# Kernel tuning notes

Hardware: AMD Instinct MI355X
Metric: run time of the kernel (lower is better)

Reference implementation:

```python
import jax, jax.numpy as jnp
import numpy as np

T, H, I, E, Z = 4096, 1024, 512, 64, 16   # tokens, hidden, intermediate, routed experts, zero experts
TOP_K = 2
SCALE = 1.5        # routed_scaling_factor
CAP = 320


def setup_inputs() -> dict:
    key = jax.random.key(0)
    k1, k2, k3, k4, k5 = jax.random.split(key, 5)
    return {
        "hidden_states": jax.random.normal(k1, (T, H), dtype=jnp.float32),
        "router_w": jax.random.normal(k2, (E + Z, H), dtype=jnp.float32) * 0.02,
        "correction_bias": jnp.zeros((E + Z,), dtype=jnp.float32),
        "w_gate": jax.random.normal(k3, (E, H, I), dtype=jnp.float32) * 0.02,
        "w_up": jax.random.normal(k4, (E, H, I), dtype=jnp.float32) * 0.02,
        "w_down": jax.random.normal(k5, (E, I, H), dtype=jnp.float32) * 0.02,
    }


def _moe_forward(hidden_states, router_w, correction_bias, w_gate, w_up, w_down):
    n_tok = hidden_states.shape[0]
    # ---- Router (fp32 gemm) ----
    logits = hidden_states @ router_w.T                      # [T, E+Z]
    scores = jax.nn.sigmoid(logits)                          # DeepSeek-V3-style sigmoid gating
    biased = scores + correction_bias[None, :]
    _, top_idx = jax.lax.top_k(biased, TOP_K)                # [T, K] selection on biased scores
    top_w = jnp.take_along_axis(scores, top_idx, axis=-1)    # weights from unbiased scores, no renorm

    # ---- Zero (identity) experts: ids >= E return the input token ----
    is_zero = top_idx >= E                                   # [T, K]
    zero_out = (top_w * is_zero).sum(-1, keepdims=True) * hidden_states

    # ---- Routed expert dispatch (capacity-based grouped GEMM) ----
    flat_e = jnp.where(is_zero, 0, top_idx).reshape(-1)      # [T*K]
    flat_w = jnp.where(is_zero, 0.0, top_w).reshape(-1)      # [T*K]
    routed_mask = (~is_zero).reshape(-1)
    oh = jax.nn.one_hot(flat_e, E, dtype=jnp.int32) * routed_mask[:, None].astype(jnp.int32)
    pos = (jnp.cumsum(oh, axis=0) * oh).sum(-1) - 1          # rank within expert; -1 for zero-expert slots
    valid = (pos >= 0) & (pos < CAP)
    pos_c = jnp.where(valid, pos, CAP)                       # overflow/zero slots -> spill row CAP
    x_rep = jnp.repeat(hidden_states, TOP_K, axis=0)         # [T*K, H]
    buf = jnp.zeros((E, CAP + 1, hidden_states.shape[1]), dtype=hidden_states.dtype)
    buf = buf.at[flat_e, pos_c].set(x_rep)[:, :CAP]          # [E, CAP, H]

    # ---- Grouped SwiGLU experts ----
    g = jax.nn.silu(jnp.einsum('ech,ehi->eci', buf, w_gate)) * jnp.einsum('ech,ehi->eci', buf, w_up)
    out_e = jnp.einsum('eci,eih->ech', g, w_down)            # [E, CAP, H]

    # ---- Combine ----
    pos_g = jnp.where(valid, pos, 0)
    y = out_e[flat_e, pos_g] * (flat_w * valid)[:, None]     # [T*K, H]
    routed = y.reshape(n_tok, TOP_K, -1).sum(1)

    return (routed + zero_out) * SCALE                       # routed_scaling_factor applied on output


def reference(hidden_states, router_w, correction_bias, w_gate, w_up, w_down):
    return _moe_forward(hidden_states, router_w, correction_bias, w_gate, w_up, w_down)
```

## Files before the change

### kernel.cpp

```cpp
#include <hip/hip_runtime.h>
#include <hip/hip_bf16.h>
#include <stdint.h>


#define T_TOK 4096
#define HDIM  1024
#define IDIM  512
#define NE    64
#define NEZ   80
#define CAPE  320
#define SCALEF 1.5f

typedef __attribute__((ext_vector_type(8))) short bf16x8;
typedef __attribute__((ext_vector_type(4))) float floatx4;

static __device__ __forceinline__ unsigned short f2bf(float f) {
    unsigned int x = __float_as_uint(f);
    x += 0x7fffu + ((x >> 16) & 1u);
    return (unsigned short)(x >> 16);
}
static __device__ __forceinline__ float bf2f(unsigned short u) {
    return __uint_as_float(((unsigned int)u) << 16);
}
static __device__ __forceinline__ uint4 pack8(const float* f) {
    uint4 v;
    asm("v_cvt_pk_bf16_f32 %0, %1, %2" : "=v"(v.x) : "v"(f[0]), "v"(f[1]));
    asm("v_cvt_pk_bf16_f32 %0, %1, %2" : "=v"(v.y) : "v"(f[2]), "v"(f[3]));
    asm("v_cvt_pk_bf16_f32 %0, %1, %2" : "=v"(v.z) : "v"(f[4]), "v"(f[5]));
    asm("v_cvt_pk_bf16_f32 %0, %1, %2" : "=v"(v.w) : "v"(f[6]), "v"(f[7]));
    return v;
}
static __device__ __forceinline__ uint2 pack4(float4 f) {
    uint2 v;
    asm("v_cvt_pk_bf16_f32 %0, %1, %2" : "=v"(v.x) : "v"(f.x), "v"(f.y));
    asm("v_cvt_pk_bf16_f32 %0, %1, %2" : "=v"(v.y) : "v"(f.z), "v"(f.w));
    return v;
}

__global__ __launch_bounds__(256) void router_kernel(
    const float* __restrict__ hidden, const float* __restrict__ rw,
    const float* __restrict__ bias, int* __restrict__ cnt,
    int* __restrict__ slot_tok, float* __restrict__ w_routed,
    float* __restrict__ zc)
{
    __shared__ float sc[8][NEZ];
    __shared__ float sbias[NEZ];
    const int tid = threadIdx.x;
    const int w = tid >> 6, lane = tid & 63;
    const int t0 = blockIdx.x * 8 + w * 2;

    if (tid < NEZ) sbias[tid] = bias[tid];

    float4 xr[2][4];
#pragma unroll
    for (int tt = 0; tt < 2; ++tt)
#pragma unroll
        for (int j4 = 0; j4 < 4; ++j4)
            xr[tt][j4] = *(const float4*)&hidden[(size_t)(t0 + tt) * HDIM + lane * 16 + j4 * 4];

    for (int eb = 0; eb < NEZ; eb += 16) {
        float acc[2][16];
#pragma unroll
        for (int tt = 0; tt < 2; ++tt)
#pragma unroll
            for (int ee = 0; ee < 16; ++ee) acc[tt][ee] = 0.f;

#pragma unroll
        for (int ee = 0; ee < 16; ++ee) {
            const float* r = rw + (size_t)(eb + ee) * HDIM + lane * 16;
#pragma unroll
            for (int j4 = 0; j4 < 4; ++j4) {
                float4 rv = *(const float4*)&r[j4 * 4];
                acc[0][ee] += xr[0][j4].x * rv.x + xr[0][j4].y * rv.y
                            + xr[0][j4].z * rv.z + xr[0][j4].w * rv.w;
                acc[1][ee] += xr[1][j4].x * rv.x + xr[1][j4].y * rv.y
                            + xr[1][j4].z * rv.z + xr[1][j4].w * rv.w;
            }
        }
#pragma unroll
        for (int off = 32; off > 0; off >>= 1)
#pragma unroll
            for (int tt = 0; tt < 2; ++tt)
#pragma unroll
                for (int ee = 0; ee < 16; ++ee)
                    acc[tt][ee] += __shfl_xor(acc[tt][ee], off);

        if (lane == 0) {
#pragma unroll
            for (int tt = 0; tt < 2; ++tt)
#pragma unroll
                for (int ee = 0; ee < 16; ++ee)
                    sc[w * 2 + tt][eb + ee] = 1.f / (1.f + __expf(-acc[tt][ee]));
        }
    }
    __syncthreads();

    if (tid < 8) {
        const int t = blockIdx.x * 8 + tid;
        float b1 = -1e30f, b2 = -1e30f; int i1 = 0, i2 = 0;
        for (int e = 0; e < NEZ; ++e) {
            float b = sc[tid][e] + sbias[e];
            if (b > b1) { b2 = b1; i2 = i1; b1 = b; i1 = e; }
            else if (b > b2) { b2 = b; i2 = e; }
        }
        float z = 0.f;
        int idx2[2] = { i1, i2 };
        for (int k = 0; k < 2; ++k) {
            int e = idx2[k];
            float wgt = sc[tid][e];
            float wr = 0.f;
            if (e >= NE) {
                z += wgt;
            } else {
                int pos = atomicAdd(&cnt[e], 1);
                if (pos < CAPE) { slot_tok[e * CAPE + pos] = t * 2 + k; wr = wgt; }
            }
            w_routed[t * 2 + k] = wr;
        }
        zc[t] = z;
    }
}

#define GU_BG 4096
#define GU_BU 8192
__global__ __launch_bounds__(256, 2) void gateup_kernel(
    const float* __restrict__ hidden,
    const float* __restrict__ w_gate, const float* __restrict__ w_up,
    const int* __restrict__ cnt, const int* __restrict__ slot_tok,
    unsigned short* __restrict__ gbuf)
{
    const int e  = blockIdx.x;
    const int n0 = blockIdx.y * 128;
    const int m0 = blockIdx.z * 128;
    int cnt_e = cnt[e]; if (cnt_e > CAPE) cnt_e = CAPE;
    if (m0 >= cnt_e) return;

    __shared__ unsigned short lds[12288];
    __shared__ int sTok[128];

    const int tid = threadIdx.x;
    const int lane = tid & 63, wid = tid >> 6;
    const int ml = lane & 15, quad = lane >> 4;
    const int wm = wid >> 1, wn = wid & 1;

    if (tid < 128) {
        int r = m0 + tid;
        sTok[tid] = (r < cnt_e) ? (slot_tok[e * CAPE + r] >> 1) : 0;
    }
    __syncthreads();

    const int ak4 = tid & 7;
    const float* ha[4];
    int aoff[4];
#pragma unroll
    for (int p = 0; p < 4; ++p) {
        int arow = (tid >> 3) + 32 * p;
        aoff[p] = (arow >> 4) * 512 + ((ak4 >> 1) * 16 + (arow & 15)) * 8 + (ak4 & 1) * 4;
        ha[p] = hidden + (size_t)sTok[arow] * HDIM + ak4 * 4;
    }
    const int bn = tid & 127, bk = tid >> 7;
    const int boff0 = (bn >> 4) * 512 + ((bk * 2) * 16 + (bn & 15)) * 8;
    const int boff1 = boff0 + 128;

    const size_t ebase = (size_t)e * HDIM * IDIM;
    const float* wg_p = w_gate + ebase + (size_t)(bk * 16) * IDIM + n0 + bn;
    const float* wu_p = w_up   + ebase + (size_t)(bk * 16) * IDIM + n0 + bn;

    float4 aR[4];
    float  gR[16], uR[16];

#pragma unroll
    for (int p = 0; p < 4; ++p) aR[p] = *(const float4*)ha[p];
#pragma unroll
    for (int jj = 0; jj < 16; ++jj) {
        gR[jj] = wg_p[(size_t)jj * IDIM];
        uR[jj] = wu_p[(size_t)jj * IDIM];
    }

    floatx4 ag[4][4], au[4][4];
#pragma unroll
    for (int mt = 0; mt < 4; ++mt)
#pragma unroll
        for (int nt = 0; nt < 4; ++nt) {
            ag[mt][nt] = (floatx4){0.f, 0.f, 0.f, 0.f};
            au[mt][nt] = (floatx4){0.f, 0.f, 0.f, 0.f};
        }

    for (int kc = 0; kc < HDIM; kc += 32) {
        {
#pragma unroll
            for (int p = 0; p < 4; ++p)
                *(uint2*)&lds[aoff[p]] = pack4(aR[p]);
            *(uint4*)&lds[GU_BG + boff0] = pack8(gR);
            *(uint4*)&lds[GU_BG + boff1] = pack8(gR + 8);
            *(uint4*)&lds[GU_BU + boff0] = pack8(uR);
            *(uint4*)&lds[GU_BU + boff1] = pack8(uR + 8);
        }
        __syncthreads();

        if (kc + 32 < HDIM) {
            wg_p += (size_t)32 * IDIM; wu_p += (size_t)32 * IDIM;
#pragma unroll
            for (int p = 0; p < 4; ++p) { ha[p] += 32; aR[p] = *(const float4*)ha[p]; }
#pragma unroll
            for (int jj = 0; jj < 16; ++jj) {
                gR[jj] = wg_p[(size_t)jj * IDIM];
                uR[jj] = wu_p[(size_t)jj * IDIM];
            }
        }

        bf16x8 a[4], bg[4], bu[4];
#pragma unroll
        for (int mt = 0; mt < 4; ++mt)
            a[mt] = *(const bf16x8*)&lds[(wm * 4 + mt) * 512 + lane * 8];
#pragma unroll
        for (int nt = 0; nt < 4; ++nt) {
            bg[nt] = *(const bf16x8*)&lds[GU_BG + (wn * 4 + nt) * 512 + lane * 8];
            bu[nt] = *(const bf16x8*)&lds[GU_BU + (wn * 4 + nt) * 512 + lane * 8];
        }
#pragma unroll
        for (int mt = 0; mt < 4; ++mt)
#pragma unroll
            for (int nt = 0; nt < 4; ++nt) {
                ag[mt][nt] = __builtin_amdgcn_mfma_f32_16x16x32_bf16(a[mt], bg[nt], ag[mt][nt], 0, 0, 0);
                au[mt][nt] = __builtin_amdgcn_mfma_f32_16x16x32_bf16(a[mt], bu[nt], au[mt][nt], 0, 0, 0);
            }
        __syncthreads();
    }

#pragma unroll
    for (int mt = 0; mt < 4; ++mt) {
#pragma unroll
        for (int r4 = 0; r4 < 4; ++r4) {
            int gm = m0 + wm * 64 + mt * 16 + quad * 4 + r4;
            if (gm < cnt_e) {
                unsigned short* grow = gbuf + (size_t)(e * CAPE + gm) * IDIM + n0 + wn * 64;
#pragma unroll
                for (int nt = 0; nt < 4; ++nt) {
                    float g = ag[mt][nt][r4];
                    float u = au[mt][nt][r4];
                    float s = g / (1.f + __expf(-g));
                    grow[nt * 16 + ml] = f2bf(s * u);
                }
            }
        }
    }
}

#define DN_B 4096
__global__ __launch_bounds__(256, 2) void down_kernel(
    const unsigned short* __restrict__ gbuf, const float* __restrict__ w_down,
    const int* __restrict__ cnt, const int* __restrict__ slot_tok,
    unsigned short* __restrict__ y2)
{
    const int e  = blockIdx.x;
    const int n0 = blockIdx.y * 128;
    const int m0 = blockIdx.z * 128;
    int cnt_e = cnt[e]; if (cnt_e > CAPE) cnt_e = CAPE;
    if (m0 >= cnt_e) return;

    __shared__ unsigned short lds[8192];
    __shared__ int sSlot[128];

    const int tid = threadIdx.x;
    const int lane = tid & 63, wid = tid >> 6;
    const int ml = lane & 15, quad = lane >> 4;
    const int wm = wid >> 1, wn = wid & 1;

    if (tid < 128) {
        int r = m0 + tid;
        sSlot[tid] = (r < cnt_e) ? slot_tok[e * CAPE + r] : 0;
    }
    __syncthreads();

    const int au8 = tid & 3;
    const unsigned short* gp[2];
    int aoff[2];
#pragma unroll
    for (int p = 0; p < 2; ++p) {
        int arow = (tid >> 2) + 64 * p;
        aoff[p] = (arow >> 4) * 512 + (au8 * 16 + (arow & 15)) * 8;
        gp[p] = gbuf + (size_t)(e * CAPE + m0 + arow) * IDIM + au8 * 8;
    }
    const int bn = tid & 127, bk = tid >> 7;
    const int boff0 = (bn >> 4) * 512 + ((bk * 2) * 16 + (bn & 15)) * 8;
    const int boff1 = boff0 + 128;
    const float* wd_p = w_down + (size_t)e * IDIM * HDIM + (size_t)(bk * 16) * HDIM + n0 + bn;

    uint4 aR[2];
    float bR[16];

#pragma unroll
    for (int p = 0; p < 2; ++p) aR[p] = *(const uint4*)gp[p];
#pragma unroll
    for (int jj = 0; jj < 16; ++jj) bR[jj] = wd_p[(size_t)jj * HDIM];

    floatx4 acc[4][4];
#pragma unroll
    for (int mt = 0; mt < 4; ++mt)
#pragma unroll
        for (int nt = 0; nt < 4; ++nt)
            acc[mt][nt] = (floatx4){0.f, 0.f, 0.f, 0.f};

    for (int kc = 0; kc < IDIM; kc += 32) {
#pragma unroll
        for (int p = 0; p < 2; ++p)
            *(uint4*)&lds[aoff[p]] = aR[p];
        *(uint4*)&lds[DN_B + boff0] = pack8(bR);
        *(uint4*)&lds[DN_B + boff1] = pack8(bR + 8);
        __syncthreads();

        if (kc + 32 < IDIM) {
            wd_p += (size_t)32 * HDIM;
#pragma unroll
            for (int p = 0; p < 2; ++p) { gp[p] += 32; aR[p] = *(const uint4*)gp[p]; }
#pragma unroll
            for (int jj = 0; jj < 16; ++jj) bR[jj] = wd_p[(size_t)jj * HDIM];
        }

        bf16x8 a[4], b[4];
#pragma unroll
        for (int mt = 0; mt < 4; ++mt)
            a[mt] = *(const bf16x8*)&lds[(wm * 4 + mt) * 512 + lane * 8];
#pragma unroll
        for (int nt = 0; nt < 4; ++nt)
            b[nt] = *(const bf16x8*)&lds[DN_B + (wn * 4 + nt) * 512 + lane * 8];
#pragma unroll
        for (int mt = 0; mt < 4; ++mt)
#pragma unroll
            for (int nt = 0; nt < 4; ++nt)
                acc[mt][nt] = __builtin_amdgcn_mfma_f32_16x16x32_bf16(a[mt], b[nt], acc[mt][nt], 0, 0, 0);
        __syncthreads();
    }

#pragma unroll
    for (int mt = 0; mt < 4; ++mt) {
#pragma unroll
        for (int r4 = 0; r4 < 4; ++r4) {
            int lrow = wm * 64 + mt * 16 + quad * 4 + r4;
            if (m0 + lrow < cnt_e) {
                int slot = sSlot[lrow];
                unsigned short* yrow = y2 + (size_t)slot * HDIM + n0 + wn * 64;
#pragma unroll
                for (int nt = 0; nt < 4; ++nt)
                    yrow[nt * 16 + ml] = f2bf(acc[mt][nt][r4]);
            }
        }
    }
}

__global__ __launch_bounds__(256) void combine_kernel(
    const float* __restrict__ hidden, const unsigned short* __restrict__ y2,
    const float* __restrict__ w_routed, const float* __restrict__ zc,
    float* __restrict__ out)
{
    int gid = blockIdx.x * 256 + threadIdx.x;
    int t = gid >> 8;
    int h = (gid & 255) * 4;
    float4 x = *(const float4*)(hidden + (size_t)t * HDIM + h);
    float w0 = w_routed[t * 2 + 0];
    float w1 = w_routed[t * 2 + 1];
    float z  = zc[t];
    ushort4 ya = *(const ushort4*)(y2 + (size_t)(t * 2 + 0) * HDIM + h);
    ushort4 yb = *(const ushort4*)(y2 + (size_t)(t * 2 + 1) * HDIM + h);
    float4 o;
    o.x = SCALEF * (z * x.x + w0 * bf2f(ya.x) + w1 * bf2f(yb.x));
    o.y = SCALEF * (z * x.y + w0 * bf2f(ya.y) + w1 * bf2f(yb.y));
    o.z = SCALEF * (z * x.z + w0 * bf2f(ya.z) + w1 * bf2f(yb.z));
    o.w = SCALEF * (z * x.w + w0 * bf2f(ya.w) + w1 * bf2f(yb.w));
    *(float4*)(out + (size_t)t * HDIM + h) = o;
}

#define OFF_CNT   0
#define OFF_SLOT  4096
#define OFF_WR    (OFF_SLOT + NE * CAPE * 4)
#define OFF_ZC    (OFF_WR + T_TOK * 2 * 4)
#define OFF_GBUF  (OFF_ZC + T_TOK * 4)
#define OFF_Y2    (OFF_GBUF + (size_t)NE * CAPE * IDIM * 2)

extern "C" void kernel_launch(void* const* d_in, const int* in_sizes, int n_in,
                              void* d_out, int out_size, void* d_ws, size_t ws_size,
                              hipStream_t stream) {
    const float* hidden = (const float*)d_in[0];
    const float* rw     = (const float*)d_in[1];
    const float* bias   = (const float*)d_in[2];
    const float* w_gate = (const float*)d_in[3];
    const float* w_up   = (const float*)d_in[4];
    const float* w_down = (const float*)d_in[5];
    float* out = (float*)d_out;

    char* ws = (char*)d_ws;
    int*   cnt      = (int*)(ws + OFF_CNT);
    int*   slot_tok = (int*)(ws + OFF_SLOT);
    float* w_rt     = (float*)(ws + OFF_WR);
    float* zc       = (float*)(ws + OFF_ZC);
    unsigned short* gbuf = (unsigned short*)(ws + OFF_GBUF);
    unsigned short* y2   = (unsigned short*)(ws + OFF_Y2);

    hipMemsetAsync(cnt, 0, NE * sizeof(int), stream);

    router_kernel<<<T_TOK / 8, 256, 0, stream>>>(hidden, rw, bias, cnt, slot_tok, w_rt, zc);

    gateup_kernel<<<dim3(NE, IDIM / 128, (CAPE + 127) / 128), 256, 0, stream>>>(
        hidden, w_gate, w_up, cnt, slot_tok, gbuf);

    down_kernel<<<dim3(NE, HDIM / 128, (CAPE + 127) / 128), 256, 0, stream>>>(
        gbuf, w_down, cnt, slot_tok, y2);

    combine_kernel<<<(T_TOK * HDIM / 4) / 256, 256, 0, stream>>>(
        hidden, y2, w_rt, zc, out);
}
```

Baseline: 483.4 us.

## Pre-convert activations to bf16 in router and halve gate/up N tile

The router kernel now writes a bf16 copy of the hidden states to a workspace buffer, and the gate/up kernel gathers tokens from it as 16-byte bf16 loads. This replaces the fp32 loads and per-iteration conversion, halving activation gather bytes. The gate/up N tile shrinks from 128 to 64 columns, doubling the grid and cutting LDS and accumulator registers to raise occupancy and parallelism, at the cost of re-reading the activations twice as often. The down kernel also clamps its A-row pointer so it never reads past the expert's capacity region.

Result: slower. 524.1 us (+8.4%).

```diff
diff --git a/kernel.cpp b/kernel.cpp
--- a/kernel.cpp
+++ b/kernel.cpp
@@ -41,7 +41,7 @@
     const float* __restrict__ hidden, const float* __restrict__ rw,
     const float* __restrict__ bias, int* __restrict__ cnt,
     int* __restrict__ slot_tok, float* __restrict__ w_routed,
-    float* __restrict__ zc)
+    float* __restrict__ zc, unsigned short* __restrict__ abuf)
 {
     __shared__ float sc[8][NEZ];
     __shared__ float sbias[NEZ];
@@ -57,6 +57,17 @@
 #pragma unroll
         for (int j4 = 0; j4 < 4; ++j4)
             xr[tt][j4] = *(const float4*)&hidden[(size_t)(t0 + tt) * HDIM + lane * 16 + j4 * 4];
+
+#pragma unroll
+    for (int tt = 0; tt < 2; ++tt) {
+        uint2 p0 = pack4(xr[tt][0]), p1 = pack4(xr[tt][1]);
+        uint2 p2 = pack4(xr[tt][2]), p3 = pack4(xr[tt][3]);
+        uint4 v0 = { p0.x, p0.y, p1.x, p1.y };
+        uint4 v1 = { p2.x, p2.y, p3.x, p3.y };
+        unsigned short* arow = abuf + (size_t)(t0 + tt) * HDIM + lane * 16;
+        *(uint4*)arow = v0;
+        *(uint4*)(arow + 8) = v1;
+    }
 
     for (int eb = 0; eb < NEZ; eb += 16) {
         float acc[2][16];
@@ -122,20 +133,20 @@
 }
 
 #define GU_BG 4096
-#define GU_BU 8192
+#define GU_BU 6144
 __global__ __launch_bounds__(256, 2) void gateup_kernel(
-    const float* __restrict__ hidden,
+    const unsigned short* __restrict__ abuf,
     const float* __restrict__ w_gate, const float* __restrict__ w_up,
     const int* __restrict__ cnt, const int* __restrict__ slot_tok,
     unsigned short* __restrict__ gbuf)
 {
     const int e  = blockIdx.x;
-    const int n0 = blockIdx.y * 128;
+    const int n0 = blockIdx.y * 64;
     const int m0 = blockIdx.z * 128;
     int cnt_e = cnt[e]; if (cnt_e > CAPE) cnt_e = CAPE;
     if (m0 >= cnt_e) return;
 
-    __shared__ unsigned short lds[12288];
+    __shared__ unsigned short lds[8192];
     __shared__ int sTok[128];
 
     const int tid = threadIdx.x;
@@ -149,39 +160,38 @@
     }
     __syncthreads();
 
-    const int ak4 = tid & 7;
-    const float* ha[4];
-    int aoff[4];
-#pragma unroll
-    for (int p = 0; p < 4; ++p) {
-        int arow = (tid >> 3) + 32 * p;
-        aoff[p] = (arow >> 4) * 512 + ((ak4 >> 1) * 16 + (arow & 15)) * 8 + (ak4 & 1) * 4;
-        ha[p] = hidden + (size_t)sTok[arow] * HDIM + ak4 * 4;
-    }
-    const int bn = tid & 127, bk = tid >> 7;
-    const int boff0 = (bn >> 4) * 512 + ((bk * 2) * 16 + (bn & 15)) * 8;
-    const int boff1 = boff0 + 128;
+    const int arow = tid >> 2, au8 = tid & 3;
+    const unsigned short* ap[2];
+    int aoff[2];
+#pragma unroll
+    for (int p = 0; p < 2; ++p) {
+        int r = arow + 64 * p;
+        aoff[p] = (r >> 4) * 512 + (au8 * 16 + (r & 15)) * 8;
+        ap[p] = abuf + (size_t)sTok[r] * HDIM + au8 * 8;
+    }
+    const int bn = tid & 63, bq = tid >> 6;
+    const int boff = (bn >> 4) * 512 + (bq * 16 + (bn & 15)) * 8;
 
     const size_t ebase = (size_t)e * HDIM * IDIM;
-    const float* wg_p = w_gate + ebase + (size_t)(bk * 16) * IDIM + n0 + bn;
-    const float* wu_p = w_up   + ebase + (size_t)(bk * 16) * IDIM + n0 + bn;
-
-    float4 aR[4];
-    float  gR[16], uR[16];
-
-#pragma unroll
-    for (int p = 0; p < 4; ++p) aR[p] = *(const float4*)ha[p];
-#pragma unroll
-    for (int jj = 0; jj < 16; ++jj) {
+    const float* wg_p = w_gate + ebase + (size_t)(bq * 8) * IDIM + n0 + bn;
+    const float* wu_p = w_up   + ebase + (size_t)(bq * 8) * IDIM + n0 + bn;
+
+    uint4 aR[2];
+    float gR[8], uR[8];
+
+#pragma unroll
+    for (int p = 0; p < 2; ++p) aR[p] = *(const uint4*)ap[p];
+#pragma unroll
+    for (int jj = 0; jj < 8; ++jj) {
         gR[jj] = wg_p[(size_t)jj * IDIM];
         uR[jj] = wu_p[(size_t)jj * IDIM];
     }
 
-    floatx4 ag[4][4], au[4][4];
+    floatx4 ag[4][2], au[4][2];
 #pragma unroll
     for (int mt = 0; mt < 4; ++mt)
 #pragma unroll
-        for (int nt = 0; nt < 4; ++nt) {
+        for (int nt = 0; nt < 2; ++nt) {
             ag[mt][nt] = (floatx4){0.f, 0.f, 0.f, 0.f};
             au[mt][nt] = (floatx4){0.f, 0.f, 0.f, 0.f};
         }
@@ -189,39 +199,37 @@
     for (int kc = 0; kc < HDIM; kc += 32) {
         {
 #pragma unroll
-            for (int p = 0; p < 4; ++p)
-                *(uint2*)&lds[aoff[p]] = pack4(aR[p]);
-            *(uint4*)&lds[GU_BG + boff0] = pack8(gR);
-            *(uint4*)&lds[GU_BG + boff1] = pack8(gR + 8);
-            *(uint4*)&lds[GU_BU + boff0] = pack8(uR);
-            *(uint4*)&lds[GU_BU + boff1] = pack8(uR + 8);
+            for (int p = 0; p < 2; ++p)
+                *(uint4*)&lds[aoff[p]] = aR[p];
+            *(uint4*)&lds[GU_BG + boff] = pack8(gR);
+            *(uint4*)&lds[GU_BU + boff] = pack8(uR);
         }
         __syncthreads();
 
         if (kc + 32 < HDIM) {
             wg_p += (size_t)32 * IDIM; wu_p += (size_t)32 * IDIM;
 #pragma unroll
-            for (int p = 0; p < 4; ++p) { ha[p] += 32; aR[p] = *(const float4*)ha[p]; }
-#pragma unroll
-            for (int jj = 0; jj < 16; ++jj) {
+            for (int p = 0; p < 2; ++p) { ap[p] += 32; aR[p] = *(const uint4*)ap[p]; }
+#pragma unroll
+            for (int jj = 0; jj < 8; ++jj) {
                 gR[jj] = wg_p[(size_t)jj * IDIM];
                 uR[jj] = wu_p[(size_t)jj * IDIM];
             }
         }
 
-        bf16x8 a[4], bg[4], bu[4];
+        bf16x8 a[4], bg[2], bu[2];
 #pragma unroll
         for (int mt = 0; mt < 4; ++mt)
             a[mt] = *(const bf16x8*)&lds[(wm * 4 + mt) * 512 + lane * 8];
 #pragma unroll
-        for (int nt = 0; nt < 4; ++nt) {
-            bg[nt] = *(const bf16x8*)&lds[GU_BG + (wn * 4 + nt) * 512 + lane * 8];
-            bu[nt] = *(const bf16x8*)&lds[GU_BU + (wn * 4 + nt) * 512 + lane * 8];
+        for (int nt = 0; nt < 2; ++nt) {
+            bg[nt] = *(const bf16x8*)&lds[GU_BG + (wn * 2 + nt) * 512 + lane * 8];
+            bu[nt] = *(const bf16x8*)&lds[GU_BU + (wn * 2 + nt) * 512 + lane * 8];
         }
 #pragma unroll
         for (int mt = 0; mt < 4; ++mt)
 #pragma unroll
-            for (int nt = 0; nt < 4; ++nt) {
+            for (int nt = 0; nt < 2; ++nt) {
                 ag[mt][nt] = __builtin_amdgcn_mfma_f32_16x16x32_bf16(a[mt], bg[nt], ag[mt][nt], 0, 0, 0);
                 au[mt][nt] = __builtin_amdgcn_mfma_f32_16x16x32_bf16(a[mt], bu[nt], au[mt][nt], 0, 0, 0);
             }
@@ -234,9 +242,9 @@
         for (int r4 = 0; r4 < 4; ++r4) {
             int gm = m0 + wm * 64 + mt * 16 + quad * 4 + r4;
             if (gm < cnt_e) {
-                unsigned short* grow = gbuf + (size_t)(e * CAPE + gm) * IDIM + n0 + wn * 64;
-#pragma unroll
-                for (int nt = 0; nt < 4; ++nt) {
+                unsigned short* grow = gbuf + (size_t)(e * CAPE + gm) * IDIM + n0 + wn * 32;
+#pragma unroll
+                for (int nt = 0; nt < 2; ++nt) {
                     float g = ag[mt][nt][r4];
                     float u = au[mt][nt][r4];
                     float s = g / (1.f + __expf(-g));
@@ -273,14 +281,15 @@
     }
     __syncthreads();
 
-    const int au8 = tid & 3;
+    const int arow = tid >> 2, au8 = tid & 3;
     const unsigned short* gp[2];
     int aoff[2];
 #pragma unroll
     for (int p = 0; p < 2; ++p) {
-        int arow = (tid >> 2) + 64 * p;
-        aoff[p] = (arow >> 4) * 512 + (au8 * 16 + (arow & 15)) * 8;
-        gp[p] = gbuf + (size_t)(e * CAPE + m0 + arow) * IDIM + au8 * 8;
+        int r = arow + 64 * p;
+        aoff[p] = (r >> 4) * 512 + (au8 * 16 + (r & 15)) * 8;
+        int rr = m0 + r; if (rr > CAPE - 1) rr = CAPE - 1;
+        gp[p] = gbuf + (size_t)(e * CAPE + rr) * IDIM + au8 * 8;
     }
     const int bn = tid & 127, bk = tid >> 7;
     const int boff0 = (bn >> 4) * 512 + ((bk * 2) * 16 + (bn & 15)) * 8;
@@ -377,6 +386,7 @@
 #define OFF_ZC    (OFF_WR + T_TOK * 2 * 4)
 #define OFF_GBUF  (OFF_ZC + T_TOK * 4)
 #define OFF_Y2    (OFF_GBUF + (size_t)NE * CAPE * IDIM * 2)
+#define OFF_ABUF  (OFF_Y2 + (size_t)T_TOK * 2 * HDIM * 2)
 
 extern "C" void kernel_launch(void* const* d_in, const int* in_sizes, int n_in,
                               void* d_out, int out_size, void* d_ws, size_t ws_size,
@@ -396,13 +406,14 @@
     float* zc       = (float*)(ws + OFF_ZC);
     unsigned short* gbuf = (unsigned short*)(ws + OFF_GBUF);
     unsigned short* y2   = (unsigned short*)(ws + OFF_Y2);
+    unsigned short* abuf = (unsigned short*)(ws + OFF_ABUF);
 
     hipMemsetAsync(cnt, 0, NE * sizeof(int), stream);
 
-    router_kernel<<<T_TOK / 8, 256, 0, stream>>>(hidden, rw, bias, cnt, slot_tok, w_rt, zc);
-
-    gateup_kernel<<<dim3(NE, IDIM / 128, (CAPE + 127) / 128), 256, 0, stream>>>(
-        hidden, w_gate, w_up, cnt, slot_tok, gbuf);
+    router_kernel<<<T_TOK / 8, 256, 0, stream>>>(hidden, rw, bias, cnt, slot_tok, w_rt, zc, abuf);
+
+    gateup_kernel<<<dim3(NE, IDIM / 64, (CAPE + 127) / 128), 256, 0, stream>>>(
+        abuf, w_gate, w_up, cnt, slot_tok, gbuf);
 
     down_kernel<<<dim3(NE, HDIM / 128, (CAPE + 127) / 128), 256, 0, stream>>>(
         gbuf, w_down, cnt, slot_tok, y2);
```
